# Optimization experiments

Measured on AMD Instinct MI355X. Metric: run time of the kernel, lower is better.

Reference implementation:

```python
import jax, jax.numpy as jnp
import numpy as np

B, S, D, H = 2, 2048, 1024, 16
DK = D // H


def setup_inputs() -> dict:
    key = jax.random.key(0)
    ks = jax.random.split(key, 11)
    s = 1.0 / np.sqrt(D)
    return {
        "q": jax.random.normal(ks[0], (B, S, D), jnp.float32),
        "k": jax.random.normal(ks[1], (B, S, D), jnp.float32),
        "v": jax.random.normal(ks[2], (B, S, D), jnp.float32),
        "mask": jnp.ones((B, 1, S, S), jnp.int32),
        "Wq": jax.random.normal(ks[3], (D, D), jnp.float32) * s,
        "bq": jnp.zeros((D,), jnp.float32),
        "Wk": jax.random.normal(ks[4], (D, D), jnp.float32) * s,
        "bk": jnp.zeros((D,), jnp.float32),
        "Wv": jax.random.normal(ks[5], (D, D), jnp.float32) * s,
        "bv": jnp.zeros((D,), jnp.float32),
        "Wo": jax.random.normal(ks[6], (D, D), jnp.float32) * s,
        "bo": jnp.zeros((D,), jnp.float32),
    }


def reference(q, k, v, mask, Wq, bq, Wk, bk, Wv, bv, Wo, bo):
    # Note: original torch code calls non-in-place masked_fill and discards the
    # result, so the mask has no mathematical effect; we preserve that.
    qh = (q @ Wq + bq).reshape(B, S, H, DK).transpose(0, 2, 1, 3)  # [B,H,S,DK]
    kh = (k @ Wk + bk).reshape(B, S, H, DK).transpose(0, 2, 1, 3)
    vh = (v @ Wv + bv).reshape(B, S, H, DK).transpose(0, 2, 1, 3)
    scores = jnp.einsum("bhqd,bhkd->bhqk", qh, kh) / jnp.sqrt(jnp.float32(DK))
    attn = jax.nn.softmax(scores, axis=-1)
    out = jnp.einsum("bhqk,bhkd->bhqd", attn, vh)  # [B,H,S,DK]
    out = out.transpose(0, 2, 1, 3).reshape(B, S, D)
    return out @ Wo + bo
```

## Files before the change

kernel.cpp:

```cpp
#include <hip/hip_runtime.h>

#define S_LEN    2048
#define D_MODEL  1024
#define N_HEADS  16
#define HEAD_DIM 64
#define BATCH    2

typedef __bf16 bf16x8 __attribute__((ext_vector_type(8)));
typedef float  floatx4 __attribute__((ext_vector_type(4)));

__device__ __forceinline__ unsigned short f2bf(float f) {
    union { float f; unsigned int u; } v;
    v.f = f;
    unsigned int u = v.u;
    u += 0x7fffu + ((u >> 16) & 1u);
    return (unsigned short)(u >> 16);
}

__device__ __forceinline__ unsigned int pk_rne(float a, float b) {
    union { float f; unsigned int u; } ua, ub;
    ua.f = a; ub.f = b;
    unsigned int x = ua.u + 0x7fffu + ((ua.u >> 16) & 1u);
    unsigned int y = ub.u + 0x7fffu + ((ub.u >> 16) & 1u);
    return __builtin_amdgcn_perm(y, x, 0x07060302);
}

__device__ __forceinline__ void gload_lds16(const unsigned short* g, unsigned short* l) {
    __builtin_amdgcn_global_load_lds(
        (const __attribute__((address_space(1))) void*)(const void*)g,
        (__attribute__((address_space(3))) void*)(void*)l,
        16, 0, 0);
}

struct PrepArgs {
    const float* src[3]; unsigned short* dst[3];
    const float* W[4];   unsigned short* Wt[4];
};

#define CONV_BLOCKS (3 * 4096)

__global__ void prep_kernel(PrepArgs args) {
    const int bid = blockIdx.x;
    if (bid < CONV_BLOCKS) {
        const int t   = bid >> 12;
        const int blk = bid & 4095;
        const int i   = blk * 256 + threadIdx.x;
        float4 f = reinterpret_cast<const float4*>(args.src[t])[i];
        ushort4 o;
        o.x = f2bf(f.x); o.y = f2bf(f.y); o.z = f2bf(f.z); o.w = f2bf(f.w);
        reinterpret_cast<ushort4*>(args.dst[t])[i] = o;
    } else {
        __shared__ unsigned short tile[64][65];
        const int r  = bid - CONV_BLOCKS;
        const int w  = r >> 8;
        const int xy = r & 255;
        const int n0 = (xy & 15) * 64, k0 = (xy >> 4) * 64;
        const float* W = args.W[w];
        unsigned short* Wt = args.Wt[w];
        for (int rep = 0; rep < 16; ++rep) {
            int e = rep * 256 + threadIdx.x;
            int kk = e >> 6, nn = e & 63;
            tile[kk][nn] = f2bf(W[(size_t)(k0 + kk) * D_MODEL + n0 + nn]);
        }
        __syncthreads();
        for (int rep = 0; rep < 16; ++rep) {
            int e = rep * 256 + threadIdx.x;
            int nn = e >> 6, kk = e & 63;
            Wt[(size_t)(n0 + nn) * D_MODEL + k0 + kk] = tile[kk][nn];
        }
    }
}

template <int TM, int TN, int MODE>
__device__ __forceinline__
void gemm_body(const unsigned short* __restrict__ A,
               const unsigned short* __restrict__ Bt,
               const float* __restrict__ bias,
               void* __restrict__ out,
               int m0, int n0, float scale,
               unsigned short* As, unsigned short* Bs) {
    constexpr int MT = TM / 32;
    constexpr int NT = TN / 32;
    const int tid  = threadIdx.x;
    const int wid  = tid >> 6;
    const int lane = tid & 63;

    floatx4 acc[MT][NT];
#pragma unroll
    for (int i = 0; i < MT; ++i)
#pragma unroll
        for (int j = 0; j < NT; ++j) acc[i][j] = (floatx4)0.0f;

    const int srow = lane >> 2;
    const int gch  = (lane & 3) ^ ((srow >> 1) & 3);
    const int wr = (wid >> 1) * (TM / 2);
    const int wc = (wid & 1) * (TN / 2);
    const int fr = lane & 15;
    const int fq = lane >> 4;
    const int swz = (fq ^ ((fr >> 1) & 3)) * 8;

    for (int k0 = 0; k0 < D_MODEL; k0 += 32) {
        if (k0) __syncthreads();
#pragma unroll
        for (int ci = 0; ci < (TM + TN) / 64; ++ci) {
            const int c = wid + ci * 4;
            if (c < TM / 16) {
                const int row = c * 16 + srow;
                gload_lds16(A + (size_t)(m0 + row) * D_MODEL + k0 + gch * 8, As + c * 512);
            } else {
                const int cb = c - TM / 16;
                const int row = cb * 16 + srow;
                gload_lds16(Bt + (size_t)(n0 + row) * D_MODEL + k0 + gch * 8, Bs + cb * 512);
            }
        }
        __syncthreads();

        bf16x8 af[MT], bfv[NT];
#pragma unroll
        for (int t = 0; t < MT; ++t)
            af[t] = *reinterpret_cast<const bf16x8*>(As + (wr + t * 16 + fr) * 32 + swz);
#pragma unroll
        for (int t = 0; t < NT; ++t)
            bfv[t] = *reinterpret_cast<const bf16x8*>(Bs + (wc + t * 16 + fr) * 32 + swz);
#pragma unroll
        for (int mt = 0; mt < MT; ++mt)
#pragma unroll
            for (int nt = 0; nt < NT; ++nt)
                acc[mt][nt] = __builtin_amdgcn_mfma_f32_16x16x32_bf16(af[mt], bfv[nt], acc[mt][nt], 0, 0, 0);
    }

#pragma unroll
    for (int nt = 0; nt < NT; ++nt) {
        const int n = n0 + wc + nt * 16 + fr;
        const float bval = bias[n];
#pragma unroll
        for (int mt = 0; mt < MT; ++mt) {
#pragma unroll
            for (int r = 0; r < 4; ++r) {
                const int m = m0 + wr + mt * 16 + fq * 4 + r;
                const float val = (acc[mt][nt][r] + bval) * scale;
                if (MODE == 2) {
                    reinterpret_cast<float*>(out)[(size_t)m * D_MODEL + n] = val;
                } else {
                    const int b = m >> 11, s = m & (S_LEN - 1);
                    const int h = n >> 6, dk = n & 63;
                    const unsigned short o16 = f2bf(val);
                    if (MODE == 0)
                        reinterpret_cast<unsigned short*>(out)[(((size_t)(b * N_HEADS + h)) * S_LEN + s) * HEAD_DIM + dk] = o16;
                    else
                        reinterpret_cast<unsigned short*>(out)[(((size_t)(b * N_HEADS + h)) * HEAD_DIM + dk) * S_LEN + s] = o16;
                }
            }
        }
    }
}

struct QKVArgs {
    const unsigned short* A[3];
    const unsigned short* Bt[3];
    const float* bias[3];
    unsigned short* out[3];
};

__global__ __launch_bounds__(256)
void qkv_gemm_kernel(QKVArgs args) {
    __shared__ __align__(16) unsigned short As[128 * 32];
    __shared__ __align__(16) unsigned short Bs[128 * 32];
    const int z = blockIdx.z;
    const int m0 = blockIdx.y * 128;
    const int n0 = blockIdx.x * 128;
    if (z == 0)
        gemm_body<128, 128, 0>(args.A[0], args.Bt[0], args.bias[0], args.out[0], m0, n0, 0.18033688011112f, As, Bs);
    else if (z == 1)
        gemm_body<128, 128, 0>(args.A[1], args.Bt[1], args.bias[1], args.out[1], m0, n0, 1.0f, As, Bs);
    else
        gemm_body<128, 128, 1>(args.A[2], args.Bt[2], args.bias[2], args.out[2], m0, n0, 1.0f, As, Bs);
}

__global__ __launch_bounds__(256)
void oproj_gemm_kernel(const unsigned short* __restrict__ A,
                       const unsigned short* __restrict__ Bt,
                       const float* __restrict__ bias,
                       float* __restrict__ out) {
    __shared__ __align__(16) unsigned short As[64 * 32];
    __shared__ __align__(16) unsigned short Bs[128 * 32];
    gemm_body<64, 128, 2>(A, Bt, bias, out, blockIdx.y * 64, blockIdx.x * 128, 1.0f, As, Bs);
}

__global__ __launch_bounds__(128)
void attn_kernel(const unsigned short* __restrict__ qhp,
                 const unsigned short* __restrict__ khp,
                 const unsigned short* __restrict__ vtp,
                 unsigned short* __restrict__ outp) {
    __shared__ __align__(16) unsigned short Qs[64 * 64];
    __shared__ __align__(16) unsigned short Ks[64 * 64];
    __shared__ __align__(16) unsigned short Vs[64 * 64];
    __shared__ __align__(16) unsigned short Ps[2][32 * 72];

    const int tid  = threadIdx.x;
    const int wid  = tid >> 6;
    const int lane = tid & 63;
    const int b = blockIdx.z, h = blockIdx.y;
    const int q0 = blockIdx.x * 64;

    const unsigned short* qbase = qhp + (size_t)(b * N_HEADS + h) * S_LEN * HEAD_DIM;
    const unsigned short* kbase = khp + (size_t)(b * N_HEADS + h) * S_LEN * HEAD_DIM;
    const unsigned short* vbase = vtp + (size_t)(b * N_HEADS + h) * HEAD_DIM * S_LEN;

    const int srow = lane >> 3;
    const int gch  = (lane & 7) ^ srow;
    const int fr = lane & 15;
    const int fq = lane >> 4;
    const int sw7 = fr & 7;

#pragma unroll
    for (int i = 0; i < 4; ++i) {
        const int c = wid * 4 + i;
        const int row = c * 8 + srow;
        gload_lds16(qbase + (size_t)(q0 + row) * HEAD_DIM + gch * 8, Qs + c * 512);
    }
    __syncthreads();

    bf16x8 qf[2][2];
#pragma unroll
    for (int qh2 = 0; qh2 < 2; ++qh2)
#pragma unroll
        for (int kk = 0; kk < 2; ++kk)
            qf[qh2][kk] = *reinterpret_cast<const bf16x8*>(
                Qs + (wid * 32 + qh2 * 16 + fr) * 64 + (((kk * 4 + fq) ^ sw7) * 8));

    floatx4 o_acc[2][4];
#pragma unroll
    for (int i = 0; i < 2; ++i)
#pragma unroll
        for (int j = 0; j < 4; ++j) o_acc[i][j] = (floatx4)0.0f;
    float l_sum[2] = {0.0f, 0.0f};

    for (int kv0 = 0; kv0 < S_LEN; kv0 += 64) {
        if (kv0) __syncthreads();
#pragma unroll
        for (int i = 0; i < 4; ++i) {
            const int c = wid * 4 + i;
            const int row = c * 8 + srow;
            gload_lds16(kbase + (size_t)(kv0 + row) * HEAD_DIM + gch * 8, Ks + c * 512);
            gload_lds16(vbase + (size_t)row * S_LEN + kv0 + gch * 8,       Vs + c * 512);
        }
        __syncthreads();

        floatx4 st[2][4];
#pragma unroll
        for (int i = 0; i < 2; ++i)
#pragma unroll
            for (int j = 0; j < 4; ++j) st[i][j] = (floatx4)0.0f;
#pragma unroll
        for (int nt = 0; nt < 4; ++nt) {
#pragma unroll
            for (int kk = 0; kk < 2; ++kk) {
                bf16x8 kf = *reinterpret_cast<const bf16x8*>(
                    Ks + (nt * 16 + fr) * 64 + (((kk * 4 + fq) ^ sw7) * 8));
                st[0][nt] = __builtin_amdgcn_mfma_f32_16x16x32_bf16(kf, qf[0][kk], st[0][nt], 0, 0, 0);
                st[1][nt] = __builtin_amdgcn_mfma_f32_16x16x32_bf16(kf, qf[1][kk], st[1][nt], 0, 0, 0);
            }
        }

#pragma unroll
        for (int qh2 = 0; qh2 < 2; ++qh2) {
#pragma unroll
            for (int nt = 0; nt < 4; ++nt) {
                float p0 = __builtin_amdgcn_exp2f(st[qh2][nt][0]);
                float p1 = __builtin_amdgcn_exp2f(st[qh2][nt][1]);
                float p2 = __builtin_amdgcn_exp2f(st[qh2][nt][2]);
                float p3 = __builtin_amdgcn_exp2f(st[qh2][nt][3]);
                l_sum[qh2] += (p0 + p1) + (p2 + p3);
                uint2 w;
                w.x = pk_rne(p0, p1);
                w.y = pk_rne(p2, p3);
                *reinterpret_cast<uint2*>(Ps[wid] + (qh2 * 16 + fr) * 72 + nt * 16 + fq * 4) = w;
            }
        }
        __asm__ volatile("s_waitcnt lgkmcnt(0)" ::: "memory");

#pragma unroll
        for (int kk = 0; kk < 2; ++kk) {
            bf16x8 pf0 = *reinterpret_cast<const bf16x8*>(Ps[wid] + (fr)      * 72 + kk * 32 + fq * 8);
            bf16x8 pf1 = *reinterpret_cast<const bf16x8*>(Ps[wid] + (16 + fr) * 72 + kk * 32 + fq * 8);
#pragma unroll
            for (int dt = 0; dt < 4; ++dt) {
                bf16x8 vf = *reinterpret_cast<const bf16x8*>(
                    Vs + (dt * 16 + fr) * 64 + (((kk * 4 + fq) ^ sw7) * 8));
                o_acc[0][dt] = __builtin_amdgcn_mfma_f32_16x16x32_bf16(pf0, vf, o_acc[0][dt], 0, 0, 0);
                o_acc[1][dt] = __builtin_amdgcn_mfma_f32_16x16x32_bf16(pf1, vf, o_acc[1][dt], 0, 0, 0);
            }
        }
    }

#pragma unroll
    for (int qh2 = 0; qh2 < 2; ++qh2) {
        float l = l_sum[qh2];
        l += __shfl_xor(l, 16);
        l += __shfl_xor(l, 32);
        float linv[4];
#pragma unroll
        for (int r = 0; r < 4; ++r)
            linv[r] = __builtin_amdgcn_rcpf(__shfl(l, fq * 4 + r));
#pragma unroll
        for (int dt = 0; dt < 4; ++dt) {
#pragma unroll
            for (int r = 0; r < 4; ++r) {
                const int s  = q0 + wid * 32 + qh2 * 16 + fq * 4 + r;
                const int dk = dt * 16 + fr;
                const float val = o_acc[qh2][dt][r] * linv[r];
                outp[((size_t)(b * S_LEN + s)) * D_MODEL + h * HEAD_DIM + dk] = f2bf(val);
            }
        }
    }
}

extern "C" void kernel_launch(void* const* d_in, const int* in_sizes, int n_in,
                              void* d_out, int out_size, void* d_ws, size_t ws_size,
                              hipStream_t stream) {
    (void)in_sizes; (void)n_in; (void)out_size; (void)ws_size;
    const float* q  = (const float*)d_in[0];
    const float* k  = (const float*)d_in[1];
    const float* v  = (const float*)d_in[2];
    const float* Wq = (const float*)d_in[4];
    const float* bq = (const float*)d_in[5];
    const float* Wk = (const float*)d_in[6];
    const float* bk = (const float*)d_in[7];
    const float* Wv = (const float*)d_in[8];
    const float* bv = (const float*)d_in[9];
    const float* Wo = (const float*)d_in[10];
    const float* bo = (const float*)d_in[11];
    float* out = (float*)d_out;

    char* ws = (char*)d_ws;
    const size_t SZ_ACT = (size_t)BATCH * S_LEN * D_MODEL * 2;
    const size_t SZ_W   = (size_t)D_MODEL * D_MODEL * 2;
    unsigned short* qb   = (unsigned short*)(ws);
    unsigned short* kb   = (unsigned short*)(ws + SZ_ACT);
    unsigned short* vb   = (unsigned short*)(ws + 2 * SZ_ACT);
    unsigned short* Wqt  = (unsigned short*)(ws + 3 * SZ_ACT);
    unsigned short* Wkt  = (unsigned short*)(ws + 3 * SZ_ACT + SZ_W);
    unsigned short* Wvt  = (unsigned short*)(ws + 3 * SZ_ACT + 2 * SZ_W);
    unsigned short* Wot  = (unsigned short*)(ws + 3 * SZ_ACT + 3 * SZ_W);
    unsigned short* qhb  = (unsigned short*)(ws + 3 * SZ_ACT + 4 * SZ_W);
    unsigned short* khb  = (unsigned short*)(ws + 4 * SZ_ACT + 4 * SZ_W);
    unsigned short* vtb  = (unsigned short*)(ws + 5 * SZ_ACT + 4 * SZ_W);
    unsigned short* attn = qb;

    PrepArgs pargs;
    pargs.src[0] = q;  pargs.src[1] = k;  pargs.src[2] = v;
    pargs.dst[0] = qb; pargs.dst[1] = kb; pargs.dst[2] = vb;
    pargs.W[0] = Wq;  pargs.W[1] = Wk;  pargs.W[2] = Wv;  pargs.W[3] = Wo;
    pargs.Wt[0] = Wqt; pargs.Wt[1] = Wkt; pargs.Wt[2] = Wvt; pargs.Wt[3] = Wot;
    prep_kernel<<<dim3(CONV_BLOCKS + 1024), 256, 0, stream>>>(pargs);

    QKVArgs gargs;
    gargs.A[0] = qb;  gargs.A[1] = kb;  gargs.A[2] = vb;
    gargs.Bt[0] = Wqt; gargs.Bt[1] = Wkt; gargs.Bt[2] = Wvt;
    gargs.bias[0] = bq; gargs.bias[1] = bk; gargs.bias[2] = bv;
    gargs.out[0] = qhb; gargs.out[1] = khb; gargs.out[2] = vtb;
    qkv_gemm_kernel<<<dim3(8, 32, 3), 256, 0, stream>>>(gargs);

    attn_kernel<<<dim3(S_LEN / 64, N_HEADS, BATCH), 128, 0, stream>>>(qhb, khb, vtb, attn);

    oproj_gemm_kernel<<<dim3(8, 64), 256, 0, stream>>>(attn, Wot, bo, out);
}
```

Baseline: 261.1 us.

## Double-buffer K/V tiles in attention and keep P in registers via permlane swaps

The attention loop now prefetches the next K/V tile into a second LDS buffer while computing on the current one, replacing the load-then-sync pattern with a single barrier per iteration. The softmax probabilities no longer round-trip through a shared P buffer. Instead, permlane32/permlane16 swaps rearrange the packed bf16 values directly into the A-operand fragment layout for the PV MFMA. The manual round-to-nearest bf16 pack is replaced by native bf16 casts. The goal is to hide global load latency and cut LDS traffic and waits. The risks are a more fragile lane permutation and a reliance on the barrier to wait for the async LDS loads.

```diff
diff --git a/kernel.cpp b/kernel.cpp
--- a/kernel.cpp
+++ b/kernel.cpp
@@ -8,6 +8,7 @@
 
 typedef __bf16 bf16x8 __attribute__((ext_vector_type(8)));
 typedef float  floatx4 __attribute__((ext_vector_type(4)));
+typedef int    intx2   __attribute__((ext_vector_type(2)));
 
 __device__ __forceinline__ unsigned short f2bf(float f) {
     union { float f; unsigned int u; } v;
@@ -17,12 +18,11 @@
     return (unsigned short)(u >> 16);
 }
 
-__device__ __forceinline__ unsigned int pk_rne(float a, float b) {
-    union { float f; unsigned int u; } ua, ub;
-    ua.f = a; ub.f = b;
-    unsigned int x = ua.u + 0x7fffu + ((ua.u >> 16) & 1u);
-    unsigned int y = ub.u + 0x7fffu + ((ub.u >> 16) & 1u);
-    return __builtin_amdgcn_perm(y, x, 0x07060302);
+__device__ __forceinline__ unsigned int pk_cvt(float a, float b) {
+    union { __bf16 h[2]; unsigned int u; } r;
+    r.h[0] = (__bf16)a;
+    r.h[1] = (__bf16)b;
+    return r.u;
 }
 
 __device__ __forceinline__ void gload_lds16(const unsigned short* g, unsigned short* l) {
@@ -192,10 +192,7 @@
                  const unsigned short* __restrict__ khp,
                  const unsigned short* __restrict__ vtp,
                  unsigned short* __restrict__ outp) {
-    __shared__ __align__(16) unsigned short Qs[64 * 64];
-    __shared__ __align__(16) unsigned short Ks[64 * 64];
-    __shared__ __align__(16) unsigned short Vs[64 * 64];
-    __shared__ __align__(16) unsigned short Ps[2][32 * 72];
+    __shared__ __align__(16) unsigned short KV[2][2][64 * 64];
 
     const int tid  = threadIdx.x;
     const int wid  = tid >> 6;
@@ -217,7 +214,9 @@
     for (int i = 0; i < 4; ++i) {
         const int c = wid * 4 + i;
         const int row = c * 8 + srow;
-        gload_lds16(qbase + (size_t)(q0 + row) * HEAD_DIM + gch * 8, Qs + c * 512);
+        gload_lds16(qbase + (size_t)(q0 + row) * HEAD_DIM + gch * 8, KV[1][0] + c * 512);
+        gload_lds16(kbase + (size_t)row * HEAD_DIM + gch * 8,        KV[0][0] + c * 512);
+        gload_lds16(vbase + (size_t)row * S_LEN + gch * 8,           KV[0][1] + c * 512);
     }
     __syncthreads();
 
@@ -227,7 +226,8 @@
 #pragma unroll
         for (int kk = 0; kk < 2; ++kk)
             qf[qh2][kk] = *reinterpret_cast<const bf16x8*>(
-                Qs + (wid * 32 + qh2 * 16 + fr) * 64 + (((kk * 4 + fq) ^ sw7) * 8));
+                KV[1][0] + (wid * 32 + qh2 * 16 + fr) * 64 + (((kk * 4 + fq) ^ sw7) * 8));
+    __syncthreads();
 
     floatx4 o_acc[2][4];
 #pragma unroll
@@ -237,15 +237,19 @@
     float l_sum[2] = {0.0f, 0.0f};
 
     for (int kv0 = 0; kv0 < S_LEN; kv0 += 64) {
-        if (kv0) __syncthreads();
-#pragma unroll
-        for (int i = 0; i < 4; ++i) {
-            const int c = wid * 4 + i;
-            const int row = c * 8 + srow;
-            gload_lds16(kbase + (size_t)(kv0 + row) * HEAD_DIM + gch * 8, Ks + c * 512);
-            gload_lds16(vbase + (size_t)row * S_LEN + kv0 + gch * 8,       Vs + c * 512);
-        }
-        __syncthreads();
+        const int cur = (kv0 >> 6) & 1;
+        if (kv0 + 64 < S_LEN) {
+            const unsigned short* kn = kbase + (size_t)(kv0 + 64) * HEAD_DIM;
+#pragma unroll
+            for (int i = 0; i < 4; ++i) {
+                const int c = wid * 4 + i;
+                const int row = c * 8 + srow;
+                gload_lds16(kn + (size_t)row * HEAD_DIM + gch * 8,                KV[cur ^ 1][0] + c * 512);
+                gload_lds16(vbase + (size_t)row * S_LEN + (kv0 + 64) + gch * 8,   KV[cur ^ 1][1] + c * 512);
+            }
+        }
+        const unsigned short* Ks = KV[cur][0];
+        const unsigned short* Vs = KV[cur][1];
 
         floatx4 st[2][4];
 #pragma unroll
@@ -263,8 +267,10 @@
             }
         }
 
+        bf16x8 pf[2][2];
 #pragma unroll
         for (int qh2 = 0; qh2 < 2; ++qh2) {
+            unsigned int u0[4], u1[4];
 #pragma unroll
             for (int nt = 0; nt < 4; ++nt) {
                 float p0 = __builtin_amdgcn_exp2f(st[qh2][nt][0]);
@@ -272,26 +278,32 @@
                 float p2 = __builtin_amdgcn_exp2f(st[qh2][nt][2]);
                 float p3 = __builtin_amdgcn_exp2f(st[qh2][nt][3]);
                 l_sum[qh2] += (p0 + p1) + (p2 + p3);
-                uint2 w;
-                w.x = pk_rne(p0, p1);
-                w.y = pk_rne(p2, p3);
-                *reinterpret_cast<uint2*>(Ps[wid] + (qh2 * 16 + fr) * 72 + nt * 16 + fq * 4) = w;
-            }
-        }
-        __asm__ volatile("s_waitcnt lgkmcnt(0)" ::: "memory");
+                u0[nt] = pk_cvt(p0, p1);
+                u1[nt] = pk_cvt(p2, p3);
+            }
+#pragma unroll
+            for (int kk = 0; kk < 2; ++kk) {
+                intx2 a  = __builtin_amdgcn_permlane32_swap((int)u0[2 * kk], (int)u0[2 * kk + 1], false, false);
+                intx2 c0 = __builtin_amdgcn_permlane16_swap(a[0], a[1], false, false);
+                intx2 bsw = __builtin_amdgcn_permlane32_swap((int)u1[2 * kk], (int)u1[2 * kk + 1], false, false);
+                intx2 c1 = __builtin_amdgcn_permlane16_swap(bsw[0], bsw[1], false, false);
+                union { int i[4]; bf16x8 v; } fb;
+                fb.i[0] = c0[0]; fb.i[1] = c1[0]; fb.i[2] = c0[1]; fb.i[3] = c1[1];
+                pf[qh2][kk] = fb.v;
+            }
+        }
 
 #pragma unroll
         for (int kk = 0; kk < 2; ++kk) {
-            bf16x8 pf0 = *reinterpret_cast<const bf16x8*>(Ps[wid] + (fr)      * 72 + kk * 32 + fq * 8);
-            bf16x8 pf1 = *reinterpret_cast<const bf16x8*>(Ps[wid] + (16 + fr) * 72 + kk * 32 + fq * 8);
 #pragma unroll
             for (int dt = 0; dt < 4; ++dt) {
                 bf16x8 vf = *reinterpret_cast<const bf16x8*>(
                     Vs + (dt * 16 + fr) * 64 + (((kk * 4 + fq) ^ sw7) * 8));
-                o_acc[0][dt] = __builtin_amdgcn_mfma_f32_16x16x32_bf16(pf0, vf, o_acc[0][dt], 0, 0, 0);
-                o_acc[1][dt] = __builtin_amdgcn_mfma_f32_16x16x32_bf16(pf1, vf, o_acc[1][dt], 0, 0, 0);
-            }
-        }
+                o_acc[0][dt] = __builtin_amdgcn_mfma_f32_16x16x32_bf16(pf[0][kk], vf, o_acc[0][dt], 0, 0, 0);
+                o_acc[1][dt] = __builtin_amdgcn_mfma_f32_16x16x32_bf16(pf[1][kk], vf, o_acc[1][dt], 0, 0, 0);
+            }
+        }
+        __syncthreads();
     }
 
 #pragma unroll
```

After: 262.5 us. About the same (+0.5%).

## Feed softmax probabilities to PV MFMA directly from registers, dropping LDS staging

Applied to the files above, without the earlier changes.

The P tile is no longer written to shared memory and read back. The exp'd scores are packed into bf16x4 register fragments whose layout matches the A operand of the 16x16x16 bf16 MFMA, and the PV product runs as 16x16x16 MFMAs with V fragments read as 4-element slices. This removes LDS writes and reads, the waitcnt, and the Ps buffer, which lowers LDS use. In exchange it issues twice as many smaller MFMAs, which may have lower throughput than the 16x16x32 variant, and it adds an inline-asm fallback with a nop fence.

```diff
diff --git a/kernel.cpp b/kernel.cpp
--- a/kernel.cpp
+++ b/kernel.cpp
@@ -8,6 +8,19 @@
 
 typedef __bf16 bf16x8 __attribute__((ext_vector_type(8)));
 typedef float  floatx4 __attribute__((ext_vector_type(4)));
+typedef short  s16x4   __attribute__((ext_vector_type(4)));
+
+#if __has_builtin(__builtin_amdgcn_mfma_f32_16x16x16bf16_1k)
+#define MFMA_PV(acc, pa, vf) acc = __builtin_amdgcn_mfma_f32_16x16x16bf16_1k(pa, vf, acc, 0, 0, 0)
+#define PV_EPILOGUE_FENCE()
+#elif __has_builtin(__builtin_amdgcn_mfma_f32_16x16x16_bf16_1k)
+#define MFMA_PV(acc, pa, vf) acc = __builtin_amdgcn_mfma_f32_16x16x16_bf16_1k(pa, vf, acc, 0, 0, 0)
+#define PV_EPILOGUE_FENCE()
+#else
+#define MFMA_PV(acc, pa, vf) \
+    asm volatile("v_mfma_f32_16x16x16_bf16 %0, %1, %2, %0" : "+v"(acc) : "v"(pa), "v"(vf))
+#define PV_EPILOGUE_FENCE() asm volatile("s_nop 7\n\ts_nop 7" ::)
+#endif
 
 __device__ __forceinline__ unsigned short f2bf(float f) {
     union { float f; unsigned int u; } v;
@@ -195,7 +208,6 @@
     __shared__ __align__(16) unsigned short Qs[64 * 64];
     __shared__ __align__(16) unsigned short Ks[64 * 64];
     __shared__ __align__(16) unsigned short Vs[64 * 64];
-    __shared__ __align__(16) unsigned short Ps[2][32 * 72];
 
     const int tid  = threadIdx.x;
     const int wid  = tid >> 6;
@@ -263,6 +275,7 @@
             }
         }
 
+        s16x4 pa[2][4];
 #pragma unroll
         for (int qh2 = 0; qh2 < 2; ++qh2) {
 #pragma unroll
@@ -272,27 +285,25 @@
                 float p2 = __builtin_amdgcn_exp2f(st[qh2][nt][2]);
                 float p3 = __builtin_amdgcn_exp2f(st[qh2][nt][3]);
                 l_sum[qh2] += (p0 + p1) + (p2 + p3);
-                uint2 w;
-                w.x = pk_rne(p0, p1);
-                w.y = pk_rne(p2, p3);
-                *reinterpret_cast<uint2*>(Ps[wid] + (qh2 * 16 + fr) * 72 + nt * 16 + fq * 4) = w;
-            }
-        }
-        __asm__ volatile("s_waitcnt lgkmcnt(0)" ::: "memory");
-
-#pragma unroll
-        for (int kk = 0; kk < 2; ++kk) {
-            bf16x8 pf0 = *reinterpret_cast<const bf16x8*>(Ps[wid] + (fr)      * 72 + kk * 32 + fq * 8);
-            bf16x8 pf1 = *reinterpret_cast<const bf16x8*>(Ps[wid] + (16 + fr) * 72 + kk * 32 + fq * 8);
+                union { unsigned int u[2]; s16x4 v; } w;
+                w.u[0] = pk_rne(p0, p1);
+                w.u[1] = pk_rne(p2, p3);
+                pa[qh2][nt] = w.v;
+            }
+        }
+
+#pragma unroll
+        for (int nt = 0; nt < 4; ++nt) {
 #pragma unroll
             for (int dt = 0; dt < 4; ++dt) {
-                bf16x8 vf = *reinterpret_cast<const bf16x8*>(
-                    Vs + (dt * 16 + fr) * 64 + (((kk * 4 + fq) ^ sw7) * 8));
-                o_acc[0][dt] = __builtin_amdgcn_mfma_f32_16x16x32_bf16(pf0, vf, o_acc[0][dt], 0, 0, 0);
-                o_acc[1][dt] = __builtin_amdgcn_mfma_f32_16x16x32_bf16(pf1, vf, o_acc[1][dt], 0, 0, 0);
-            }
-        }
-    }
+                s16x4 vf = *reinterpret_cast<const s16x4*>(
+                    Vs + (dt * 16 + fr) * 64 + (((2 * nt + (fq >> 1)) ^ sw7) * 8) + (fq & 1) * 4);
+                MFMA_PV(o_acc[0][dt], pa[0][nt], vf);
+                MFMA_PV(o_acc[1][dt], pa[1][nt], vf);
+            }
+        }
+    }
+    PV_EPILOGUE_FENCE();
 
 #pragma unroll
     for (int qh2 = 0; qh2 < 2; ++qh2) {
```

After: 272.4 us. +4.3%, slower.
